# Kernel tuning notes

Hardware: AMD Instinct MI355X
Metric: run time of the kernel (lower is better)

Reference implementation:

```python
import jax, jax.numpy as jnp
import numpy as np

B, L, D, E, K, P = 1024, 320, 128, 8, 2, 96
NOISE_EPS = 0.01
LOSS_COEF = 0.01


def setup_inputs() -> dict:
    key = jax.random.key(0)
    ks = jax.random.split(key, 8)
    return {
        "x": jax.random.normal(ks[0], (B, L, D), jnp.float32),
        "x_mark_enc": jax.random.normal(ks[1], (B, L, 4), jnp.float32),
        "noise": jax.random.normal(ks[2], (B, E), jnp.float32),  # randn_like in torch
        "start_w": jax.random.normal(ks[3], (D, 1), jnp.float32) * 0.05,
        "start_b": jnp.zeros((1,), jnp.float32),
        "w_gate": jax.random.normal(ks[4], (L, E), jnp.float32) * 0.02,
        "w_noise": jax.random.normal(ks[5], (L, E), jnp.float32) * 0.02,
        "expert_w": jax.random.normal(ks[6], (E, L, P), jnp.float32) * (1.0 / np.sqrt(L)),
        "expert_b": jnp.zeros((E, P, D), jnp.float32),
    }


def _norm_cdf(v):
    return 0.5 * (1.0 + jax.lax.erf(v * (1.0 / np.sqrt(2.0)).astype(v.dtype) if hasattr((1.0 / np.sqrt(2.0)), 'astype') else v / jnp.sqrt(jnp.asarray(2.0, v.dtype))))


def _cdf(v):
    # standard normal CDF, Normal(0,1).cdf
    return 0.5 * (1.0 + jax.lax.erf(v / jnp.sqrt(jnp.asarray(2.0, v.dtype))))


def _cv_squared(v):
    eps = 1e-10
    return jnp.var(v, ddof=1) / (jnp.mean(v) ** 2 + eps)


def reference(x, x_mark_enc, noise, start_w, start_b, w_gate, w_noise, expert_b, expert_w):
    # --- noisy top-k gating (train mode) ---
    g = jnp.squeeze(x @ start_w, -1) + start_b  # [B, L]
    clean_logits = g @ w_gate                    # [B, E]
    noise_std = jax.nn.softplus(g @ w_noise) + NOISE_EPS
    noisy_logits = clean_logits + noise * noise_std

    top_logits, top_idx = jax.lax.top_k(noisy_logits, K + 1)  # [B, K+1]
    top_k_gates = jax.nn.softmax(top_logits[:, :K], axis=1)
    gates = jnp.zeros_like(noisy_logits).at[
        jnp.arange(noisy_logits.shape[0])[:, None], top_idx[:, :K]
    ].set(top_k_gates)  # [B, E] sparse gates (zeros elsewhere)

    # --- differentiable load via prob-in-top-k ---
    thr_in = top_logits[:, K:K + 1]       # (k+1)-th noisy value
    thr_out = top_logits[:, K - 1:K]      # k-th noisy value
    clean_c = jnp.where(jnp.isnan(clean_logits), 0.0, clean_logits)
    prob = jnp.where(
        noisy_logits > thr_in,
        _cdf((clean_c - thr_in) / noise_std),
        _cdf((clean_c - thr_out) / noise_std),
    )
    load = prob.sum(0)          # [E]
    importance = gates.sum(0)   # [E]
    balance_loss = LOSS_COEF * (_cv_squared(importance) + _cv_squared(load))

    # --- dispatch/combine: dense-equivalent of SparseDispatcher ---
    # expert e: out_e = einsum('bld,lp->bpd', x, W_e); combine weights = gates
    per_expert = jnp.einsum('bld,elp->ebpd', x, expert_w)          # [E, B, P, D]
    out = jnp.einsum('be,ebpd->bpd', gates, per_expert)
    out = out + jnp.einsum('be,epd->bpd', gates, expert_b)
    regu_sum = jnp.asarray(0.0, jnp.float32)
    return out, balance_loss, regu_sum
```

## Files before the change

kernel.cpp:

```cpp
#include <hip/hip_runtime.h>
#include <hip/hip_bf16.h>

#define Bn 1024
#define Lr 320
#define Dd 128
#define Ee 8
#define Pp 96

typedef short bf16x8 __attribute__((ext_vector_type(8)));
typedef float f32x4 __attribute__((ext_vector_type(4)));
typedef unsigned u32x4 __attribute__((ext_vector_type(4)));
typedef unsigned short u16;

__device__ __forceinline__ float cdf_f(float v) {
    return 0.5f * (1.0f + erff(v * 0.70710678118654752f));
}
__device__ __forceinline__ float softplus_f(float x) {
    return fmaxf(x, 0.0f) + log1pf(expf(-fabsf(x)));
}
__device__ __forceinline__ u16 f2bf(float f) {
    unsigned int u = __float_as_uint(f);
    return (u16)((u + 0x7fffu + ((u >> 16) & 1u)) >> 16);
}
__device__ __forceinline__ float bf2f(u16 u) {
    return __uint_as_float(((unsigned int)u) << 16);
}

__device__ __forceinline__ void gload16(const void* g, void* l) {
    __builtin_amdgcn_global_load_lds(
        (const __attribute__((address_space(1))) void*)g,
        (__attribute__((address_space(3))) void*)l, 16, 0, 0);
}

__global__ __launch_bounds__(256) void transpose_w(
    const float* __restrict__ ew, u16* __restrict__ wt,
    float* __restrict__ accum, float* __restrict__ zbuf)
{
    __shared__ float tile[Pp * 33];
    const int e  = blockIdx.x;
    const int l0 = blockIdx.y * 32;
    const int t  = threadIdx.x;
    if (e == 0 && blockIdx.y == 0 && t < 16) accum[t] = 0.f;
    {
        const int idx = (blockIdx.x * 10 + blockIdx.y) * 256 + t;
        if (idx < Bn * 16) zbuf[idx] = 0.f;
    }
    #pragma unroll
    for (int i = 0; i < 12; ++i) {
        const int idx = t + 256 * i;
        const int lp = idx / 96, p = idx - 96 * lp;
        tile[p * 33 + lp] = ew[((size_t)e * Lr + l0 + lp) * Pp + p];
    }
    __syncthreads();
    #pragma unroll
    for (int i = 0; i < 6; ++i) {
        const int g = t + 256 * i;
        const int p = g >> 4, l2 = (g & 15) * 2;
        const unsigned pk = (unsigned)f2bf(tile[p * 33 + l2]) |
                            ((unsigned)f2bf(tile[p * 33 + l2 + 1]) << 16);
        *(unsigned*)&wt[((size_t)(e * Pp + p)) * Lr + l0 + l2] = pk;
    }
}

__global__ __launch_bounds__(256, 8) void g2_kernel(
    const float* __restrict__ x, const float* __restrict__ start_w,
    const float* __restrict__ start_b, const float* __restrict__ w_gate,
    const float* __restrict__ w_noise, float* __restrict__ zbuf)
{
    __shared__ float sred[16];
    const int t  = threadIdx.x;
    const int lc = blockIdx.x;
    const int b  = blockIdx.y;
    const float sb = start_b[0];
    const int f8 = t & 7;

    if (t < 16) sred[t] = 0.f;
    __syncthreads();

    float4 sw[4];
    #pragma unroll
    for (int j = 0; j < 4; ++j) sw[j] = ((const float4*)start_w)[f8 + 8 * j];

    const float* xb = x + ((size_t)b * Lr + lc * 64) * Dd;
    float zc = 0.f, zn = 0.f;
    #pragma unroll
    for (int p2 = 0; p2 < 2; ++p2) {
        const int r = p2 * 32 + (t >> 3);
        float acc = 0.f;
        #pragma unroll
        for (int j = 0; j < 4; ++j) {
            const float4 v = ((const float4*)(xb + (size_t)r * Dd))[f8 + 8 * j];
            acc += v.x * sw[j].x + v.y * sw[j].y + v.z * sw[j].z + v.w * sw[j].w;
        }
        #pragma unroll
        for (int off = 1; off <= 4; off <<= 1) acc += __shfl_xor(acc, off);
        const float gv = acc + sb;
        const int l = lc * 64 + r;
        zc += gv * w_gate[l * Ee + f8];
        zn += gv * w_noise[l * Ee + f8];
    }
    #pragma unroll
    for (int off = 8; off <= 32; off <<= 1) {
        zc += __shfl_xor(zc, off);
        zn += __shfl_xor(zn, off);
    }
    if ((t & 63) < 8) {
        atomicAdd(&sred[f8], zc);
        atomicAdd(&sred[8 + f8], zn);
    }
    __syncthreads();
    if (t < 16) atomicAdd(&zbuf[b * 16 + t], sred[t]);
}

__global__ __launch_bounds__(256) void topk_kernel(
    const float* __restrict__ zbuf, const float* __restrict__ noise,
    float* __restrict__ accum, float* __restrict__ gates_out)
{
    __shared__ float sred[16];
    const int t = threadIdx.x;
    const int b = blockIdx.x * 256 + t;

    if (t < 16) sred[t] = 0.f;
    __syncthreads();

    float zc[8], zn[8], nsy[8], sdv[8];
    #pragma unroll
    for (int e = 0; e < 8; ++e) {
        zc[e] = zbuf[b * 16 + e];
        zn[e] = zbuf[b * 16 + 8 + e];
    }
    #pragma unroll
    for (int e = 0; e < 8; ++e) {
        sdv[e] = softplus_f(zn[e]) + 0.01f;
        nsy[e] = zc[e] + noise[b * Ee + e] * sdv[e];
    }

    int i0 = -1, i1 = -1;
    float v0 = -INFINITY, v1 = -INFINITY, v2 = -INFINITY;
    #pragma unroll
    for (int i = 0; i < 8; ++i) if (nsy[i] > v0) { v0 = nsy[i]; i0 = i; }
    #pragma unroll
    for (int i = 0; i < 8; ++i) if (i != i0 && nsy[i] > v1) { v1 = nsy[i]; i1 = i; }
    #pragma unroll
    for (int i = 0; i < 8; ++i) if (i != i0 && i != i1 && nsy[i] > v2) { v2 = nsy[i]; }

    const float ex1 = expf(v1 - v0);
    const float den = 1.f + ex1;
    const float g0 = 1.f / den, g1 = ex1 / den;

    float im[8], pr[8];
    #pragma unroll
    for (int e = 0; e < 8; ++e) {
        im[e] = (e == i0) ? g0 : ((e == i1) ? g1 : 0.f);
        float c = zc[e];
        if (isnan(c)) c = 0.f;
        pr[e] = (nsy[e] > v2) ? cdf_f((c - v2) / sdv[e])
                              : cdf_f((c - v1) / sdv[e]);
        gates_out[b * Ee + e] = im[e];
    }

    #pragma unroll
    for (int off = 1; off <= 32; off <<= 1) {
        #pragma unroll
        for (int e = 0; e < 8; ++e) {
            pr[e] += __shfl_xor(pr[e], off);
            im[e] += __shfl_xor(im[e], off);
        }
    }
    if ((t & 63) == 0) {
        #pragma unroll
        for (int e = 0; e < 8; ++e) {
            atomicAdd(&sred[e], pr[e]);
            atomicAdd(&sred[8 + e], im[e]);
        }
    }
    __syncthreads();
    if (t < 16) atomicAdd(&accum[t], sred[t]);
}

__global__ __launch_bounds__(256, 4) void mm_kernel(
    const float* __restrict__ x, const u16* __restrict__ wt,
    const float* __restrict__ expert_b, const float* __restrict__ gates,
    const float* __restrict__ accum, float* __restrict__ out)
{
    __shared__ __align__(16) unsigned Ws[2][192 * 16];

    const int tid  = threadIdx.x;

    if (blockIdx.x == 0 && tid == 0) {
        float lo[8], im[8];
        #pragma unroll
        for (int i = 0; i < 8; ++i) { lo[i] = accum[i]; im[i] = accum[8 + i]; }
        float ml = 0.f, mi = 0.f;
        #pragma unroll
        for (int i = 0; i < 8; ++i) { ml += lo[i]; mi += im[i]; }
        ml *= 0.125f; mi *= 0.125f;
        float sl = 0.f, si = 0.f;
        #pragma unroll
        for (int i = 0; i < 8; ++i) {
            const float dl = lo[i] - ml, di = im[i] - mi;
            sl += dl * dl; si += di * di;
        }
        const float cvl = (sl / 7.f) / (ml * ml + 1e-10f);
        const float cvi = (si / 7.f) / (mi * mi + 1e-10f);
        float* os = out + (size_t)Bn * Pp * Dd;
        os[0] = 0.01f * (cvi + cvl);
        os[1] = 0.0f;
    }

    const int b    = blockIdx.x >> 1;
    const int h    = blockIdx.x & 1;
    const int lane = tid & 63;
    const int wv   = tid >> 6;
    const int quad = lane >> 4;
    const int r16  = lane & 15;

    int e0 = 0, e1 = 0; float g0 = 0.f, g1 = 0.f; int cnt = 0;
    #pragma unroll
    for (int e = 0; e < Ee; ++e) {
        const float gv = gates[b * Ee + e];
        if (gv != 0.f) {
            if (cnt == 0) { e0 = e; g0 = gv; }
            else if (cnt == 1) { e1 = e; g1 = gv; }
            ++cnt;
        }
    }

    const u16* w0r = wt + (size_t)e0 * Pp * Lr;
    const u16* w1r = wt + (size_t)e1 * Pp * Lr;

    const int d = h * 64 + 16 * wv + r16;
    const float* xg = x + ((size_t)b * Lr + 8 * quad) * Dd + d;

    const int wrow = lane >> 2;
    const int wq   = lane & 3;

    auto STAGE_W = [&](int buf, int l0) {
        #pragma unroll
        for (int i = 0; i < 3; ++i) {
            const int c  = 3 * wv + i;
            const int r  = 16 * c + wrow;
            const int dw = (4 * wq) ^ ((r & 3) << 2);
            const u16* src = (c < 6) ? (w0r + (size_t)r * Lr)
                                     : (w1r + (size_t)(r - 96) * Lr);
            gload16(src + l0 + 2 * dw, (void*)&Ws[buf][c * 256]);
        }
    };

    float xa[8], xb8[8];
    auto LOADX = [&](float* dst, int l0) {
        #pragma unroll
        for (int k = 0; k < 8; ++k)
            dst[k] = xg[(size_t)(l0 + k) * Dd];
    };

    f32x4 a0[6], a1[6];
    #pragma unroll
    for (int m = 0; m < 6; ++m) {
        a0[m] = (f32x4){0.f, 0.f, 0.f, 0.f};
        a1[m] = (f32x4){0.f, 0.f, 0.f, 0.f};
    }

    const int wdw = (4 * quad) ^ ((r16 & 3) << 2);

    union UF { u32x4 q; bf16x8 v; unsigned u[4]; };

    auto COMPUTE = [&](int buf, const float* xv) {
        UF xf;
        #pragma unroll
        for (int k2 = 0; k2 < 4; ++k2)
            xf.u[k2] = (unsigned)f2bf(xv[2 * k2]) |
                       ((unsigned)f2bf(xv[2 * k2 + 1]) << 16);
        #pragma unroll
        for (int m = 0; m < 6; ++m) {
            UF f0, f1;
            f0.q = *(const u32x4*)&Ws[buf][(16 * m + r16) * 16 + wdw];
            f1.q = *(const u32x4*)&Ws[buf][(96 + 16 * m + r16) * 16 + wdw];
            a0[m] = __builtin_amdgcn_mfma_f32_16x16x32_bf16(f0.v, xf.v, a0[m], 0, 0, 0);
            a1[m] = __builtin_amdgcn_mfma_f32_16x16x32_bf16(f1.v, xf.v, a1[m], 0, 0, 0);
        }
    };

    STAGE_W(0, 0);
    LOADX(xa, 0);
    __syncthreads();

    #pragma unroll
    for (int t = 0; t < 10; t += 2) {
        STAGE_W(1, 32 * (t + 1));
        LOADX(xb8, 32 * (t + 1));
        COMPUTE(0, xa);
        __syncthreads();
        if (t + 2 < 10) {
            STAGE_W(0, 32 * (t + 2));
            LOADX(xa, 32 * (t + 2));
        }
        COMPUTE(1, xb8);
        __syncthreads();
    }

    const float* eb0 = expert_b + (size_t)e0 * Pp * Dd;
    const float* eb1 = expert_b + (size_t)e1 * Pp * Dd;
    #pragma unroll
    for (int m = 0; m < 6; ++m) {
        #pragma unroll
        for (int r = 0; r < 4; ++r) {
            const int p = 16 * m + 4 * quad + r;
            out[((size_t)b * Pp + p) * Dd + d] =
                g0 * (a0[m][r] + eb0[p * Dd + d]) +
                g1 * (a1[m][r] + eb1[p * Dd + d]);
        }
    }
}

extern "C" void kernel_launch(void* const* d_in, const int* in_sizes, int n_in,
                              void* d_out, int out_size, void* d_ws, size_t ws_size,
                              hipStream_t stream)
{
    const float* x        = (const float*)d_in[0];
    const float* noise    = (const float*)d_in[2];
    const float* start_w  = (const float*)d_in[3];
    const float* start_b  = (const float*)d_in[4];
    const float* w_gate   = (const float*)d_in[5];
    const float* w_noise  = (const float*)d_in[6];
    const float* expert_w = (const float*)d_in[7];
    const float* expert_b = (const float*)d_in[8];
    float* out            = (float*)d_out;

    float* accum = (float*)d_ws;
    float* gates = accum + 16;
    float* zbuf  = gates + Bn * Ee;
    u16*   wt    = (u16*)(zbuf + Bn * 16);

    hipLaunchKernelGGL(transpose_w, dim3(Ee, Lr / 32), dim3(256), 0, stream,
                       expert_w, wt, accum, zbuf);
    hipLaunchKernelGGL(g2_kernel, dim3(5, Bn), dim3(256), 0, stream,
                       x, start_w, start_b, w_gate, w_noise, zbuf);
    hipLaunchKernelGGL(topk_kernel, dim3(Bn / 256), dim3(256), 0, stream,
                       zbuf, noise, accum, gates);
    hipLaunchKernelGGL(mm_kernel, dim3(Bn * 2), dim3(256), 0, stream,
                       x, wt, expert_b, gates, accum, out);
}
```

Before: 306.2 us.

## Fuse weight transpose into top-k kernel, drop atomics, widen matmul blocks

Removes the separate transpose/zero-init kernel by folding the weight transpose into extra blocks of the top-k kernel. The gating partial sums and loss statistics are now written to per-block slots and reduced by the consumer instead of accumulated with global atomics, so no zero-initialisation is needed. The matmul kernel now uses one 512-thread block per batch row covering both D halves, so the shared weight tile is staged once per row instead of twice. This saves a launch and duplicate weight staging, at the cost of more zbuf traffic and lower occupancy per block.

```diff
diff --git a/kernel.cpp b/kernel.cpp
--- a/kernel.cpp
+++ b/kernel.cpp
@@ -30,36 +30,6 @@
     __builtin_amdgcn_global_load_lds(
         (const __attribute__((address_space(1))) void*)g,
         (__attribute__((address_space(3))) void*)l, 16, 0, 0);
-}
-
-__global__ __launch_bounds__(256) void transpose_w(
-    const float* __restrict__ ew, u16* __restrict__ wt,
-    float* __restrict__ accum, float* __restrict__ zbuf)
-{
-    __shared__ float tile[Pp * 33];
-    const int e  = blockIdx.x;
-    const int l0 = blockIdx.y * 32;
-    const int t  = threadIdx.x;
-    if (e == 0 && blockIdx.y == 0 && t < 16) accum[t] = 0.f;
-    {
-        const int idx = (blockIdx.x * 10 + blockIdx.y) * 256 + t;
-        if (idx < Bn * 16) zbuf[idx] = 0.f;
-    }
-    #pragma unroll
-    for (int i = 0; i < 12; ++i) {
-        const int idx = t + 256 * i;
-        const int lp = idx / 96, p = idx - 96 * lp;
-        tile[p * 33 + lp] = ew[((size_t)e * Lr + l0 + lp) * Pp + p];
-    }
-    __syncthreads();
-    #pragma unroll
-    for (int i = 0; i < 6; ++i) {
-        const int g = t + 256 * i;
-        const int p = g >> 4, l2 = (g & 15) * 2;
-        const unsigned pk = (unsigned)f2bf(tile[p * 33 + l2]) |
-                            ((unsigned)f2bf(tile[p * 33 + l2 + 1]) << 16);
-        *(unsigned*)&wt[((size_t)(e * Pp + p)) * Lr + l0 + l2] = pk;
-    }
 }
 
 __global__ __launch_bounds__(256, 8) void g2_kernel(
@@ -109,15 +79,40 @@
         atomicAdd(&sred[8 + f8], zn);
     }
     __syncthreads();
-    if (t < 16) atomicAdd(&zbuf[b * 16 + t], sred[t]);
-}
-
-__global__ __launch_bounds__(256) void topk_kernel(
+    if (t < 16) zbuf[(b * 5 + lc) * 16 + t] = sred[t];
+}
+
+__global__ __launch_bounds__(256) void tk_tr_kernel(
     const float* __restrict__ zbuf, const float* __restrict__ noise,
-    float* __restrict__ accum, float* __restrict__ gates_out)
+    const float* __restrict__ ew, u16* __restrict__ wt,
+    float* __restrict__ lossbuf, float* __restrict__ gates_out)
 {
-    __shared__ float sred[16];
+    __shared__ float tile[Pp * 33];
     const int t = threadIdx.x;
+
+    if (blockIdx.x >= 4) {
+        const int bx = blockIdx.x - 4;
+        const int e  = bx / 10;
+        const int l0 = (bx - 10 * e) * 32;
+        #pragma unroll
+        for (int i = 0; i < 12; ++i) {
+            const int idx = t + 256 * i;
+            const int lp = idx / 96, p = idx - 96 * lp;
+            tile[p * 33 + lp] = ew[((size_t)e * Lr + l0 + lp) * Pp + p];
+        }
+        __syncthreads();
+        #pragma unroll
+        for (int i = 0; i < 6; ++i) {
+            const int g = t + 256 * i;
+            const int p = g >> 4, l2 = (g & 15) * 2;
+            const unsigned pk = (unsigned)f2bf(tile[p * 33 + l2]) |
+                                ((unsigned)f2bf(tile[p * 33 + l2 + 1]) << 16);
+            *(unsigned*)&wt[((size_t)(e * Pp + p)) * Lr + l0 + l2] = pk;
+        }
+        return;
+    }
+
+    float* sred = tile;
     const int b = blockIdx.x * 256 + t;
 
     if (t < 16) sred[t] = 0.f;
@@ -125,9 +120,14 @@
 
     float zc[8], zn[8], nsy[8], sdv[8];
     #pragma unroll
-    for (int e = 0; e < 8; ++e) {
-        zc[e] = zbuf[b * 16 + e];
-        zn[e] = zbuf[b * 16 + 8 + e];
+    for (int e = 0; e < 8; ++e) { zc[e] = 0.f; zn[e] = 0.f; }
+    #pragma unroll
+    for (int lc = 0; lc < 5; ++lc) {
+        #pragma unroll
+        for (int e = 0; e < 8; ++e) {
+            zc[e] += zbuf[(b * 5 + lc) * 16 + e];
+            zn[e] += zbuf[(b * 5 + lc) * 16 + 8 + e];
+        }
     }
     #pragma unroll
     for (int e = 0; e < 8; ++e) {
@@ -175,22 +175,27 @@
         }
     }
     __syncthreads();
-    if (t < 16) atomicAdd(&accum[t], sred[t]);
-}
-
-__global__ __launch_bounds__(256, 4) void mm_kernel(
+    if (t < 16) lossbuf[blockIdx.x * 16 + t] = sred[t];
+}
+
+__global__ __launch_bounds__(512, 2) void mm_kernel(
     const float* __restrict__ x, const u16* __restrict__ wt,
     const float* __restrict__ expert_b, const float* __restrict__ gates,
-    const float* __restrict__ accum, float* __restrict__ out)
+    const float* __restrict__ lossbuf, float* __restrict__ out)
 {
     __shared__ __align__(16) unsigned Ws[2][192 * 16];
 
-    const int tid  = threadIdx.x;
+    const int tid = threadIdx.x;
 
     if (blockIdx.x == 0 && tid == 0) {
         float lo[8], im[8];
         #pragma unroll
-        for (int i = 0; i < 8; ++i) { lo[i] = accum[i]; im[i] = accum[8 + i]; }
+        for (int i = 0; i < 8; ++i) {
+            lo[i] = lossbuf[i]      + lossbuf[16 + i] +
+                    lossbuf[32 + i] + lossbuf[48 + i];
+            im[i] = lossbuf[8 + i]  + lossbuf[24 + i] +
+                    lossbuf[40 + i] + lossbuf[56 + i];
+        }
         float ml = 0.f, mi = 0.f;
         #pragma unroll
         for (int i = 0; i < 8; ++i) { ml += lo[i]; mi += im[i]; }
@@ -208,10 +213,11 @@
         os[1] = 0.0f;
     }
 
-    const int b    = blockIdx.x >> 1;
-    const int h    = blockIdx.x & 1;
+    const int b    = blockIdx.x;
     const int lane = tid & 63;
     const int wv   = tid >> 6;
+    const int hh   = wv >> 2;
+    const int nt   = wv & 3;
     const int quad = lane >> 4;
     const int r16  = lane & 15;
 
@@ -229,20 +235,26 @@
     const u16* w0r = wt + (size_t)e0 * Pp * Lr;
     const u16* w1r = wt + (size_t)e1 * Pp * Lr;
 
-    const int d = h * 64 + 16 * wv + r16;
+    const int d = hh * 64 + nt * 16 + r16;
     const float* xg = x + ((size_t)b * Lr + 8 * quad) * Dd + d;
 
     const int wrow = lane >> 2;
     const int wq   = lane & 3;
 
     auto STAGE_W = [&](int buf, int l0) {
-        #pragma unroll
-        for (int i = 0; i < 3; ++i) {
-            const int c  = 3 * wv + i;
+        {
+            const int c  = wv;
             const int r  = 16 * c + wrow;
             const int dw = (4 * wq) ^ ((r & 3) << 2);
             const u16* src = (c < 6) ? (w0r + (size_t)r * Lr)
                                      : (w1r + (size_t)(r - 96) * Lr);
+            gload16(src + l0 + 2 * dw, (void*)&Ws[buf][c * 256]);
+        }
+        if (wv < 4) {
+            const int c  = 8 + wv;
+            const int r  = 16 * c + wrow;
+            const int dw = (4 * wq) ^ ((r & 3) << 2);
+            const u16* src = w1r + (size_t)(r - 96) * Lr;
             gload16(src + l0 + 2 * dw, (void*)&Ws[buf][c * 256]);
         }
     };
@@ -327,17 +339,15 @@
     const float* expert_b = (const float*)d_in[8];
     float* out            = (float*)d_out;
 
-    float* accum = (float*)d_ws;
-    float* gates = accum + 16;
-    float* zbuf  = gates + Bn * Ee;
-    u16*   wt    = (u16*)(zbuf + Bn * 16);
-
-    hipLaunchKernelGGL(transpose_w, dim3(Ee, Lr / 32), dim3(256), 0, stream,
-                       expert_w, wt, accum, zbuf);
+    float* gates   = (float*)d_ws;
+    float* zbuf    = gates + Bn * Ee;
+    float* lossbuf = zbuf + Bn * 80;
+    u16*   wt      = (u16*)(lossbuf + 64);
+
     hipLaunchKernelGGL(g2_kernel, dim3(5, Bn), dim3(256), 0, stream,
                        x, start_w, start_b, w_gate, w_noise, zbuf);
-    hipLaunchKernelGGL(topk_kernel, dim3(Bn / 256), dim3(256), 0, stream,
-                       zbuf, noise, accum, gates);
-    hipLaunchKernelGGL(mm_kernel, dim3(Bn * 2), dim3(256), 0, stream,
-                       x, wt, expert_b, gates, accum, out);
-}
+    hipLaunchKernelGGL(tk_tr_kernel, dim3(84), dim3(256), 0, stream,
+                       zbuf, noise, expert_w, wt, lossbuf, gates);
+    hipLaunchKernelGGL(mm_kernel, dim3(Bn), dim3(512), 0, stream,
+                       x, wt, expert_b, gates, lossbuf, out);
+}
```

Result: no change. 300.6 us (-1.8%).
